# Kernel optimization log

Hardware: AMD Instinct MI355X
Metric: run time of the kernel (lower is better)

## Reference

```python
import jax, jax.numpy as jnp
import numpy as np

EPS = 1e-8


def setup_inputs() -> dict:
    key = jax.random.key(0)
    k1, k2, k3 = jax.random.split(key, 3)
    B, K, L, D = 4, 64, 128, 768
    context = jax.random.normal(k1, (B, K, 2, L, D), dtype=jnp.float32)
    # MlpModule(input_size=D): Linear(D, D) -> ReLU -> Linear(D, 1)
    w1 = jax.random.normal(k2, (D, D), dtype=jnp.float32) * (1.0 / np.sqrt(D))
    b1 = jnp.zeros((D,), dtype=jnp.float32)
    w2 = jax.random.normal(k3, (D, 1), dtype=jnp.float32) * (1.0 / np.sqrt(D))
    b2 = jnp.zeros((1,), dtype=jnp.float32)
    return {"context": context, "w1": w1, "b1": b1, "w2": w2, "b2": b2}


def reference(context, w1, b1, w2, b2):
    # context: [B, K, 2, L, D]; slice 0 = context tokens, slice 1 = entity tokens
    ctx = context[:, :, 0, :, :]   # [B, K, L, D]
    ent = context[:, :, 1, :, :]   # [B, K, L, D]

    ctx_norm = jnp.linalg.norm(ctx, axis=-1, keepdims=True)  # [B, K, L, 1]
    ent_norm = jnp.linalg.norm(ent, axis=-1, keepdims=True)  # [B, K, L, 1]

    # cosine-similarity score matrix: [B, K, L, L]
    denom = ctx_norm * jnp.swapaxes(ent_norm, -1, -2) + EPS
    scores = jnp.einsum('bkld,bkmd->bklm', ctx, ent) / denom

    # normalized embeddings (torch code does in-place /= before the stack)
    ctx_n = ctx / ctx_norm
    ent_n = ent / ent_norm

    # top-1 match along entity axis, gather matched entity token per context token
    argmax_idx = jnp.argmax(scores, axis=-1)                       # [B, K, L] int
    matched = jnp.take_along_axis(ent_n, argmax_idx[..., None], axis=2)  # [B, K, L, D]

    pair = jnp.stack([ctx_n, matched], axis=-2)  # [B, K, L, 2, D]

    # MLP: Linear(D,D) -> ReLU -> Linear(D,1), then sum over the pair axis
    h = jax.nn.relu(jnp.einsum('bklpd,de->bklpe', pair, w1) + b1)
    out = jnp.einsum('bklpd,do->bklpo', h, w2) + b2   # [B, K, L, 2, 1]
    out = jnp.sum(out, axis=-2)                        # [B, K, L, 1]
    return jnp.squeeze(out, axis=-1)                   # [B, K, L]
```

## Files before the change

### kernel.cpp

```cpp
#include <hip/hip_runtime.h>
#include <hip/hip_bf16.h>
#include <stdint.h>

#define NB 4
#define NK 64
#define NL 128
#define ND 768
#define NBK (NB*NK)
#define NROW (NBK*NL)
#define LD2 (NL*ND)
#define EPSF 1e-8f
#define THETA 2e-3f
#define CAP 16384

#define TSTR 40

typedef __bf16 bf16x8 __attribute__((ext_vector_type(8)));
typedef float  f32x4  __attribute__((ext_vector_type(4)));

__device__ __forceinline__ int row_off(int r) {
  if (r < NROW) return r*ND + (r >> 7)*LD2;
  int r2 = r - NROW;
  return r2*ND + (r2 >> 7)*LD2 + LD2;
}

__global__ __launch_bounds__(256) void k0_w1t(const float* __restrict__ w1,
                                              __bf16* __restrict__ w1t,
                                              unsigned long long* __restrict__ amax2,
                                              unsigned* __restrict__ cntg) {
  __shared__ float tile[64][68];
  int idx = blockIdx.x*256 + threadIdx.x;
  if (idx < NROW) amax2[idx] = 0ull;
  if (idx == 0) *cntg = 0u;
  int kb = (blockIdx.x / 12) * 64, eb = (blockIdx.x % 12) * 64;
  int t = threadIdx.x;
  int r = t >> 2, c0 = (t & 3) * 16;
  #pragma unroll
  for (int j = 0; j < 4; j++) {
    f32x4 v = *(const f32x4*)(w1 + (kb + r)*ND + eb + c0 + j*4);
    *(f32x4*)&tile[r][c0 + j*4] = v;
  }
  __syncthreads();
  int e = t & 63, gi = t >> 6;
  int eg = eb + e;
  #pragma unroll
  for (int g2 = 0; g2 < 2; g2++) {
    int g = gi*2 + g2;
    bf16x8 o;
    #pragma unroll
    for (int j = 0; j < 8; j++) o[j] = (__bf16)tile[g*8 + j][e];
    int G = (kb >> 3) + (g ^ (eg & 7));
    *(bf16x8*)(w1t + eg*ND + G*8) = o;
  }
}

__device__ __forceinline__ void cvt4(f32x4 v, unsigned& hp0, unsigned& hp1,
                                     unsigned& lp0, unsigned& lp1, float& sq) {
  unsigned u0 = __float_as_uint(v[0]), u1 = __float_as_uint(v[1]);
  unsigned u2 = __float_as_uint(v[2]), u3 = __float_as_uint(v[3]);
  hp0 = (u1 & 0xffff0000u) | (u0 >> 16);
  hp1 = (u3 & 0xffff0000u) | (u2 >> 16);
  float l0 = v[0] - __uint_as_float(u0 & 0xffff0000u);
  float l1 = v[1] - __uint_as_float(u1 & 0xffff0000u);
  float l2 = v[2] - __uint_as_float(u2 & 0xffff0000u);
  float l3 = v[3] - __uint_as_float(u3 & 0xffff0000u);
  lp0 = (__float_as_uint(l1) & 0xffff0000u) | (__float_as_uint(l0) >> 16);
  lp1 = (__float_as_uint(l3) & 0xffff0000u) | (__float_as_uint(l2) >> 16);
  sq += v[0]*v[0] + v[1]*v[1] + v[2]*v[2] + v[3]*v[3];
}

__device__ __forceinline__ bf16x8 rnd8(f32x4 a, f32x4 b) {
  bf16x8 o;
  o[0] = (__bf16)a[0]; o[1] = (__bf16)a[1]; o[2] = (__bf16)a[2]; o[3] = (__bf16)a[3];
  o[4] = (__bf16)b[0]; o[5] = (__bf16)b[1]; o[6] = (__bf16)b[2]; o[7] = (__bf16)b[3];
  return o;
}

__global__ __launch_bounds__(512) void k2a_screen(
    const float* __restrict__ ctxall, float* __restrict__ norm,
    int* __restrict__ amax, unsigned* __restrict__ cntg,
    unsigned* __restrict__ list, __bf16* __restrict__ abf16) {
  __shared__ alignas(16) __bf16 tiles[2][4][128*TSTR];
  __shared__ float einv_s[128];
  int bk = blockIdx.x;
  int t = threadIdx.x;
  int mat = t >> 8, row = (t >> 1) & 127, kh = (t & 1) * 16;
  const float* src = ctxall + bk*2*LD2 + mat*LD2 + row*ND + kh;
  int w = t >> 6, lane = t & 63, quad = lane >> 4, eloc = lane & 15;
  __bf16* arow = abf16 ? (abf16 + (size_t)((mat ? NROW : 0) + bk*NL + row)*ND + kh)
                       : (__bf16*)0;

  f32x4 pv[4];
  #pragma unroll
  for (int i = 0; i < 4; i++) pv[i] = *(const f32x4*)(src + i*4);
  float sq = 0.f;
  f32x4 acc[8];
  #pragma unroll
  for (int ct = 0; ct < 8; ct++) acc[ct] = (f32x4){0,0,0,0};

  int p = 0;
  for (int kt = 0; kt < 24; kt++) {
    unsigned h0,h1,h2,h3, l0,l1,l2,l3;
    cvt4(pv[0], h0, h1, l0, l1, sq);
    cvt4(pv[1], h2, h3, l2, l3, sq);
    __bf16* hdst = &tiles[p][2*mat  ][row*TSTR + kh];
    __bf16* ldst = &tiles[p][2*mat+1][row*TSTR + kh];
    *(uint4*)hdst = make_uint4(h0,h1,h2,h3);
    *(uint4*)ldst = make_uint4(l0,l1,l2,l3);
    bf16x8 rb0, rb1;
    if (arow) rb0 = rnd8(pv[0], pv[1]);
    cvt4(pv[2], h0, h1, l0, l1, sq);
    cvt4(pv[3], h2, h3, l2, l3, sq);
    *((uint4*)hdst + 1) = make_uint4(h0,h1,h2,h3);
    *((uint4*)ldst + 1) = make_uint4(l0,l1,l2,l3);
    if (arow) rb1 = rnd8(pv[2], pv[3]);
    __syncthreads();
    if (arow) {
      *(bf16x8*)(arow + kt*32) = rb0;
      *(bf16x8*)(arow + kt*32 + 8) = rb1;
    }
    if (kt < 23) {
      const float* s2 = src + (kt+1)*32;
      #pragma unroll
      for (int i = 0; i < 4; i++) pv[i] = *(const f32x4*)(s2 + i*4);
    }
    bf16x8 ah = *(const bf16x8*)&tiles[p][0][(w*16+eloc)*TSTR + quad*8];
    bf16x8 al = *(const bf16x8*)&tiles[p][1][(w*16+eloc)*TSTR + quad*8];
    #pragma unroll
    for (int ct = 0; ct < 8; ct++) {
      bf16x8 bh = *(const bf16x8*)&tiles[p][2][(ct*16+eloc)*TSTR + quad*8];
      bf16x8 bl = *(const bf16x8*)&tiles[p][3][(ct*16+eloc)*TSTR + quad*8];
      acc[ct] = __builtin_amdgcn_mfma_f32_16x16x32_bf16(al, bh, acc[ct], 0, 0, 0);
      acc[ct] = __builtin_amdgcn_mfma_f32_16x16x32_bf16(ah, bl, acc[ct], 0, 0, 0);
      acc[ct] = __builtin_amdgcn_mfma_f32_16x16x32_bf16(ah, bh, acc[ct], 0, 0, 0);
    }
    p ^= 1;
  }

  float stot = sq + __shfl_xor(sq, 1);
  if ((t & 1) == 0) {
    float n = sqrtf(stot);
    if (mat == 0) norm[bk*NL + row] = n;
    else { norm[NROW + bk*NL + row] = n; einv_s[row] = 1.0f / n; }
  }
  __syncthreads();

  #pragma unroll
  for (int rr = 0; rr < 4; rr++) {
    float sc[8];
    float best = -3.0e38f; int bcol = 0;
    #pragma unroll
    for (int ct = 0; ct < 8; ct++) {
      sc[ct] = acc[ct][rr] * einv_s[ct*16 + eloc];
      int col = ct*16 + eloc;
      if (sc[ct] > best) { best = sc[ct]; bcol = col; }
    }
    #pragma unroll
    for (int m = 1; m < 16; m <<= 1) {
      float ov = __shfl_xor(best, m);
      int   oc = __shfl_xor(bcol, m);
      if (ov > best || (ov == best && oc < bcol)) { best = ov; bcol = oc; }
    }
    int grow = bk*NL + w*16 + quad*4 + rr;
    if (eloc == 0) amax[grow] = bcol;
    int cnt = 0;
    #pragma unroll
    for (int ct = 0; ct < 8; ct++) cnt += (sc[ct] >= best - THETA) ? 1 : 0;
    #pragma unroll
    for (int m = 1; m < 16; m <<= 1) cnt += __shfl_xor(cnt, m);
    if (cnt >= 2) {
      #pragma unroll
      for (int ct = 0; ct < 8; ct++) {
        if (sc[ct] >= best - THETA) {
          unsigned idx = atomicAdd(cntg, 1u);
          if (idx < CAP) list[idx] = ((unsigned)grow << 7) | (unsigned)(ct*16 + eloc);
        }
      }
    }
  }
}

__global__ __launch_bounds__(256) void k2b_rescore(
    const float* __restrict__ ctxall, const float* __restrict__ norm,
    const unsigned* __restrict__ cntg, const unsigned* __restrict__ list,
    unsigned long long* __restrict__ amax2) {
  unsigned n = *cntg; if (n > CAP) n = CAP;
  int lane = threadIdx.x & 63;
  unsigned wv = blockIdx.x*4 + (threadIdx.x >> 6);
  for (unsigned e = wv; e < n; e += 256) {
    unsigned ent = list[e];
    int row = (int)(ent >> 7), col = (int)(ent & 127);
    int bk = row >> 7;
    const float* a = ctxall + row_off(row);
    const float* b = ctxall + bk*2*LD2 + LD2 + col*ND;
    float d = 0.f;
    #pragma unroll
    for (int i = 0; i < 3; i++) {
      f32x4 va = *(const f32x4*)(a + lane*12 + i*4);
      f32x4 vb = *(const f32x4*)(b + lane*12 + i*4);
      d += va[0]*vb[0] + va[1]*vb[1] + va[2]*vb[2] + va[3]*vb[3];
    }
    #pragma unroll
    for (int m = 1; m < 64; m <<= 1) d += __shfl_xor(d, m);
    if (lane == 0) {
      float cn = norm[row], en = norm[NROW + bk*NL + col];
      float s = d / (cn*en + EPSF);
      unsigned su = __float_as_uint(s);
      unsigned ord = (su & 0x80000000u) ? ~su : (su | 0x80000000u);
      unsigned long long key = ((unsigned long long)ord << 32) | (unsigned)(127 - col);
      atomicMax(&amax2[row], key);
    }
  }
}

__global__ __launch_bounds__(256, 2) void k3_mlp_b(
    const __bf16* __restrict__ abf16, const float* __restrict__ norm,
    const __bf16* __restrict__ w1t, const float* __restrict__ b1,
    const float* __restrict__ w2, float* __restrict__ val) {
  __shared__ alignas(16) __bf16 btile[2][16*768];
  int tid = threadIdx.x;
  int wave = tid >> 6, lane = tid & 63;
  int quad = lane >> 4, eloc = lane & 15;
  int rbase = blockIdx.x*128 + wave*32;

  #pragma unroll
  for (int i = 0; i < 6; i++) {
    __builtin_amdgcn_global_load_lds(
      (const __attribute__((address_space(1))) unsigned int*)(w1t + (i*256 + tid)*8),
      (__attribute__((address_space(3))) unsigned int*)(&btile[0][0] + (i*256 + tid)*8),
      16, 0, 0);
  }

  bf16x8 afrag[2][24];
  float rinvv[2][4];
  #pragma unroll
  for (int s = 0; s < 2; s++) {
    const __bf16* src = abf16 + (size_t)(rbase + s*16 + eloc)*ND + quad*8;
    #pragma unroll
    for (int ks = 0; ks < 24; ks++)
      afrag[s][ks] = *(const bf16x8*)(src + ks*32);
    #pragma unroll
    for (int rr = 0; rr < 4; rr++)
      rinvv[s][rr] = 1.0f / norm[rbase + s*16 + quad*4 + rr];
  }

  float oacc[2][4] = {{0,0,0,0},{0,0,0,0}};
  int p = 0;
  for (int nt = 0; nt < 48; nt++) {
    __syncthreads();
    if (nt < 47) {
      const __bf16* gsrc = w1t + (nt+1)*16*ND;
      #pragma unroll
      for (int i = 0; i < 6; i++) {
        __builtin_amdgcn_global_load_lds(
          (const __attribute__((address_space(1))) unsigned int*)(gsrc + (i*256 + tid)*8),
          (__attribute__((address_space(3))) unsigned int*)(&btile[p^1][0] + (i*256 + tid)*8),
          16, 0, 0);
      }
    }
    f32x4 h0 = {0,0,0,0}, h1 = {0,0,0,0};
    #pragma unroll
    for (int ks = 0; ks < 24; ks++) {
      int g = ks*4 + quad;
      bf16x8 bfrag = *(const bf16x8*)(&btile[p][0] + eloc*ND + ((g ^ (eloc & 7))*8));
      h0 = __builtin_amdgcn_mfma_f32_16x16x32_bf16(afrag[0][ks], bfrag, h0, 0, 0, 0);
      h1 = __builtin_amdgcn_mfma_f32_16x16x32_bf16(afrag[1][ks], bfrag, h1, 0, 0, 0);
    }
    float b1v = b1[nt*16 + eloc];
    float w2v = w2[nt*16 + eloc];
    #pragma unroll
    for (int rr = 0; rr < 4; rr++) {
      oacc[0][rr] += fmaxf(h0[rr]*rinvv[0][rr] + b1v, 0.f) * w2v;
      oacc[1][rr] += fmaxf(h1[rr]*rinvv[1][rr] + b1v, 0.f) * w2v;
    }
    p ^= 1;
  }
  #pragma unroll
  for (int m = 1; m < 16; m <<= 1)
    #pragma unroll
    for (int s = 0; s < 2; s++)
      #pragma unroll
      for (int rr = 0; rr < 4; rr++)
        oacc[s][rr] += __shfl_xor(oacc[s][rr], m);
  if (eloc == 0) {
    #pragma unroll
    for (int s = 0; s < 2; s++)
      #pragma unroll
      for (int rr = 0; rr < 4; rr++)
        val[rbase + s*16 + quad*4 + rr] = oacc[s][rr];
  }
}

__global__ __launch_bounds__(256, 2) void k3_mlp(
    const float* __restrict__ ctxall, const float* __restrict__ norm,
    const __bf16* __restrict__ w1t, const float* __restrict__ b1,
    const float* __restrict__ w2, float* __restrict__ val) {
  __shared__ alignas(16) __bf16 btile[2][16*768];
  int tid = threadIdx.x;
  int wave = tid >> 6, lane = tid & 63;
  int quad = lane >> 4, eloc = lane & 15;
  int rbase = blockIdx.x*128 + wave*32;

  #pragma unroll
  for (int i = 0; i < 6; i++) {
    __builtin_amdgcn_global_load_lds(
      (const __attribute__((address_space(1))) unsigned int*)(w1t + (i*256 + tid)*8),
      (__attribute__((address_space(3))) unsigned int*)(&btile[0][0] + (i*256 + tid)*8),
      16, 0, 0);
  }

  bf16x8 afrag[2][24];
  #pragma unroll
  for (int s = 0; s < 2; s++) {
    int r = rbase + s*16 + eloc;
    const float* src = ctxall + row_off(r);
    float rinv = 1.0f / norm[r];
    #pragma unroll
    for (int ks = 0; ks < 24; ks++) {
      const float* sp = src + ks*32 + quad*8;
      f32x4 v0 = *(const f32x4*)sp;
      f32x4 v1 = *(const f32x4*)(sp + 4);
      bf16x8 a;
      a[0] = (__bf16)(v0[0]*rinv); a[1] = (__bf16)(v0[1]*rinv);
      a[2] = (__bf16)(v0[2]*rinv); a[3] = (__bf16)(v0[3]*rinv);
      a[4] = (__bf16)(v1[0]*rinv); a[5] = (__bf16)(v1[1]*rinv);
      a[6] = (__bf16)(v1[2]*rinv); a[7] = (__bf16)(v1[3]*rinv);
      afrag[s][ks] = a;
    }
  }

  float oacc[2][4] = {{0,0,0,0},{0,0,0,0}};
  int p = 0;
  for (int nt = 0; nt < 48; nt++) {
    __syncthreads();
    if (nt < 47) {
      const __bf16* gsrc = w1t + (nt+1)*16*ND;
      #pragma unroll
      for (int i = 0; i < 6; i++) {
        __builtin_amdgcn_global_load_lds(
          (const __attribute__((address_space(1))) unsigned int*)(gsrc + (i*256 + tid)*8),
          (__attribute__((address_space(3))) unsigned int*)(&btile[p^1][0] + (i*256 + tid)*8),
          16, 0, 0);
      }
    }
    f32x4 h0 = {0,0,0,0}, h1 = {0,0,0,0};
    #pragma unroll
    for (int ks = 0; ks < 24; ks++) {
      int g = ks*4 + quad;
      bf16x8 bfrag = *(const bf16x8*)(&btile[p][0] + eloc*ND + ((g ^ (eloc & 7))*8));
      h0 = __builtin_amdgcn_mfma_f32_16x16x32_bf16(afrag[0][ks], bfrag, h0, 0, 0, 0);
      h1 = __builtin_amdgcn_mfma_f32_16x16x32_bf16(afrag[1][ks], bfrag, h1, 0, 0, 0);
    }
    float b1v = b1[nt*16 + eloc];
    float w2v = w2[nt*16 + eloc];
    #pragma unroll
    for (int rr = 0; rr < 4; rr++) {
      oacc[0][rr] += fmaxf(h0[rr] + b1v, 0.f) * w2v;
      oacc[1][rr] += fmaxf(h1[rr] + b1v, 0.f) * w2v;
    }
    p ^= 1;
  }
  #pragma unroll
  for (int m = 1; m < 16; m <<= 1)
    #pragma unroll
    for (int s = 0; s < 2; s++)
      #pragma unroll
      for (int rr = 0; rr < 4; rr++)
        oacc[s][rr] += __shfl_xor(oacc[s][rr], m);
  if (eloc == 0) {
    #pragma unroll
    for (int s = 0; s < 2; s++)
      #pragma unroll
      for (int rr = 0; rr < 4; rr++)
        val[rbase + s*16 + quad*4 + rr] = oacc[s][rr];
  }
}

__global__ void k4_out(const float* __restrict__ val, const int* __restrict__ amax,
                       const unsigned long long* __restrict__ amax2,
                       const float* __restrict__ b2, float* __restrict__ out) {
  int i = blockIdx.x*256 + threadIdx.x;
  int bk = i >> 7;
  unsigned long long k = amax2[i];
  int a = k ? (127 - (int)(k & 127ull)) : amax[i];
  out[i] = val[i] + val[NROW + bk*NL + a] + 2.0f*b2[0];
}

extern "C" void kernel_launch(void* const* d_in, const int* in_sizes, int n_in,
                              void* d_out, int out_size, void* d_ws, size_t ws_size,
                              hipStream_t stream) {
  const float* ctxall = (const float*)d_in[0];
  const float* w1 = (const float*)d_in[1];
  const float* b1 = (const float*)d_in[2];
  const float* w2 = (const float*)d_in[3];
  const float* b2 = (const float*)d_in[4];
  float* out = (float*)d_out;

  char* ws = (char*)d_ws;
  float*    norm = (float*)ws;
  int*      amax = (int*)(ws + 262144);
  float*    val  = (float*)(ws + 393216);
  __bf16*   w1t  = (__bf16*)(ws + 655360);
  unsigned long long* amax2 = (unsigned long long*)(ws + 1835008);
  unsigned* cntg = (unsigned*)(ws + 2097152);
  unsigned* list = (unsigned*)(ws + 2097156);

  const size_t abf_off = 8ull << 20;
  const size_t abf_bytes = (size_t)2*NROW*ND*sizeof(__bf16);
  __bf16* abf16 = (ws_size >= abf_off + abf_bytes) ? (__bf16*)(ws + abf_off)
                                                   : (__bf16*)0;

  hipLaunchKernelGGL(k0_w1t,     dim3(144),        dim3(256), 0, stream, w1, w1t, amax2, cntg);
  hipLaunchKernelGGL(k2a_screen, dim3(NBK),        dim3(512), 0, stream, ctxall, norm, amax, cntg, list, abf16);
  hipLaunchKernelGGL(k2b_rescore,dim3(64),         dim3(256), 0, stream, ctxall, norm, cntg, list, amax2);
  if (abf16) {
    hipLaunchKernelGGL(k3_mlp_b, dim3(2*NROW/128), dim3(256), 0, stream, abf16, norm, w1t, b1, w2, val);
  } else {
    hipLaunchKernelGGL(k3_mlp,   dim3(2*NROW/128), dim3(256), 0, stream, ctxall, norm, w1t, b1, w2, val);
  }
  hipLaunchKernelGGL(k4_out,     dim3(NROW/256),   dim3(256), 0, stream, val, amax, amax2, b2, out);
}
```

Before: 441.2 us.

## Restructure bf16 MLP kernel to stream activations through LDS and hold W1 per wave

The bf16 MLP kernel is rewritten with 512 threads. Each of 8 waves owns 96 output columns, and W1 fragments are read straight from global memory (L2). The 128 activation rows are streamed through double-buffered LDS in 32-wide K slices, where before W1 tiles were streamed through LDS and A was held in registers. Accumulators for all 128 rows by 96 columns live in registers (48 f32x4 per lane), and a cross-wave LDS reduction then forms the final score. This aims to cut the redundant streaming of W1 per block and improve MFMA density, but adds heavy register pressure, per-k-step barriers and uncached W1 global loads.

```diff
diff --git a/kernel.cpp b/kernel.cpp
--- a/kernel.cpp
+++ b/kernel.cpp
@@ -12,7 +12,6 @@
 #define EPSF 1e-8f
 #define THETA 2e-3f
 #define CAP 16384
-
 #define TSTR 40
 
 typedef __bf16 bf16x8 __attribute__((ext_vector_type(8)));
@@ -213,81 +212,109 @@
   }
 }
 
-__global__ __launch_bounds__(256, 2) void k3_mlp_b(
+__global__ __launch_bounds__(512, 2) void k3_mlp_c(
     const __bf16* __restrict__ abf16, const float* __restrict__ norm,
     const __bf16* __restrict__ w1t, const float* __restrict__ b1,
     const float* __restrict__ w2, float* __restrict__ val) {
-  __shared__ alignas(16) __bf16 btile[2][16*768];
+  __shared__ alignas(16) __bf16 atile[2][128*32];
+  __shared__ float red[8][128];
   int tid = threadIdx.x;
   int wave = tid >> 6, lane = tid & 63;
   int quad = lane >> 4, eloc = lane & 15;
-  int rbase = blockIdx.x*128 + wave*32;
-
+  int rbase = blockIdx.x * 128;
+  int arow = tid >> 2, acol = (tid & 3) * 8;
+
+  {
+    const __bf16* s0 = abf16 + (size_t)(rbase + arow)*ND + acol;
+    __builtin_amdgcn_global_load_lds(
+      (const __attribute__((address_space(1))) unsigned int*)s0,
+      (__attribute__((address_space(3))) unsigned int*)(&atile[0][0] + tid*8),
+      16, 0, 0);
+  }
+
+  float b1v[6], w2v[6];
   #pragma unroll
   for (int i = 0; i < 6; i++) {
-    __builtin_amdgcn_global_load_lds(
-      (const __attribute__((address_space(1))) unsigned int*)(w1t + (i*256 + tid)*8),
-      (__attribute__((address_space(3))) unsigned int*)(&btile[0][0] + (i*256 + tid)*8),
-      16, 0, 0);
-  }
-
-  bf16x8 afrag[2][24];
-  float rinvv[2][4];
-  #pragma unroll
-  for (int s = 0; s < 2; s++) {
-    const __bf16* src = abf16 + (size_t)(rbase + s*16 + eloc)*ND + quad*8;
-    #pragma unroll
-    for (int ks = 0; ks < 24; ks++)
-      afrag[s][ks] = *(const bf16x8*)(src + ks*32);
-    #pragma unroll
-    for (int rr = 0; rr < 4; rr++)
-      rinvv[s][rr] = 1.0f / norm[rbase + s*16 + quad*4 + rr];
-  }
-
-  float oacc[2][4] = {{0,0,0,0},{0,0,0,0}};
+    int out = (wave + 8*i)*16 + eloc;
+    b1v[i] = b1[out];
+    w2v[i] = w2[out];
+  }
+
+  f32x4 acc[6][8];
+  #pragma unroll
+  for (int i = 0; i < 6; i++)
+    #pragma unroll
+    for (int rt = 0; rt < 8; rt++) acc[i][rt] = (f32x4){0,0,0,0};
+
   int p = 0;
-  for (int nt = 0; nt < 48; nt++) {
+  for (int ksp = 0; ksp < 12; ksp++) {
+    int ks0 = ksp*2;
     __syncthreads();
-    if (nt < 47) {
-      const __bf16* gsrc = w1t + (nt+1)*16*ND;
-      #pragma unroll
-      for (int i = 0; i < 6; i++) {
-        __builtin_amdgcn_global_load_lds(
-          (const __attribute__((address_space(1))) unsigned int*)(gsrc + (i*256 + tid)*8),
-          (__attribute__((address_space(3))) unsigned int*)(&btile[p^1][0] + (i*256 + tid)*8),
-          16, 0, 0);
-      }
-    }
-    f32x4 h0 = {0,0,0,0}, h1 = {0,0,0,0};
-    #pragma unroll
-    for (int ks = 0; ks < 24; ks++) {
-      int g = ks*4 + quad;
-      bf16x8 bfrag = *(const bf16x8*)(&btile[p][0] + eloc*ND + ((g ^ (eloc & 7))*8));
-      h0 = __builtin_amdgcn_mfma_f32_16x16x32_bf16(afrag[0][ks], bfrag, h0, 0, 0, 0);
-      h1 = __builtin_amdgcn_mfma_f32_16x16x32_bf16(afrag[1][ks], bfrag, h1, 0, 0, 0);
-    }
-    float b1v = b1[nt*16 + eloc];
-    float w2v = w2[nt*16 + eloc];
-    #pragma unroll
-    for (int rr = 0; rr < 4; rr++) {
-      oacc[0][rr] += fmaxf(h0[rr]*rinvv[0][rr] + b1v, 0.f) * w2v;
-      oacc[1][rr] += fmaxf(h1[rr]*rinvv[1][rr] + b1v, 0.f) * w2v;
+    {
+      const __bf16* s1 = abf16 + (size_t)(rbase + arow)*ND + (ks0+1)*32 + acol;
+      __builtin_amdgcn_global_load_lds(
+        (const __attribute__((address_space(1))) unsigned int*)s1,
+        (__attribute__((address_space(3))) unsigned int*)(&atile[p^1][0] + tid*8),
+        16, 0, 0);
+    }
+    bf16x8 bf0[6], bf1[6];
+    #pragma unroll
+    for (int i = 0; i < 6; i++) {
+      const __bf16* brow = w1t + ((wave + 8*i)*16 + eloc)*ND;
+      int g0 = ks0*4 + quad;
+      bf0[i] = *(const bf16x8*)(brow + ((g0       ^ (eloc & 7))*8));
+      bf1[i] = *(const bf16x8*)(brow + (((g0 + 4) ^ (eloc & 7))*8));
+    }
+    #pragma unroll
+    for (int rt = 0; rt < 8; rt++) {
+      bf16x8 af = *(const bf16x8*)&atile[p][(rt*16 + eloc)*32 + quad*8];
+      #pragma unroll
+      for (int i = 0; i < 6; i++)
+        acc[i][rt] = __builtin_amdgcn_mfma_f32_16x16x32_bf16(af, bf0[i], acc[i][rt], 0, 0, 0);
     }
     p ^= 1;
-  }
-  #pragma unroll
-  for (int m = 1; m < 16; m <<= 1)
-    #pragma unroll
-    for (int s = 0; s < 2; s++)
-      #pragma unroll
-      for (int rr = 0; rr < 4; rr++)
-        oacc[s][rr] += __shfl_xor(oacc[s][rr], m);
-  if (eloc == 0) {
-    #pragma unroll
-    for (int s = 0; s < 2; s++)
-      #pragma unroll
-      for (int rr = 0; rr < 4; rr++)
-        val[rbase + s*16 + quad*4 + rr] = oacc[s][rr];
+    __syncthreads();
+    if (ksp < 11) {
+      const __bf16* s2 = abf16 + (size_t)(rbase + arow)*ND + (ks0+2)*32 + acol;
+      __builtin_amdgcn_global_load_lds(
+        (const __attribute__((address_space(1))) unsigned int*)s2,
+        (__attribute__((address_space(3))) unsigned int*)(&atile[p^1][0] + tid*8),
+        16, 0, 0);
+    }
+    #pragma unroll
+    for (int rt = 0; rt < 8; rt++) {
+      bf16x8 af = *(const bf16x8*)&atile[p][(rt*16 + eloc)*32 + quad*8];
+      #pragma unroll
+      for (int i = 0; i < 6; i++)
+        acc[i][rt] = __builtin_amdgcn_mfma_f32_16x16x32_bf16(af, bf1[i], acc[i][rt], 0, 0, 0);
+    }
+    p ^= 1;
+  }
+
+  #pragma unroll
+  for (int rt = 0; rt < 8; rt++) {
+    f32x4 nv = *(const f32x4*)&norm[rbase + rt*16 + quad*4];
+    f32x4 rv;
+    #pragma unroll
+    for (int r = 0; r < 4; r++) rv[r] = 1.0f / nv[r];
+    f32x4 s = {0,0,0,0};
+    #pragma unroll
+    for (int i = 0; i < 6; i++)
+      #pragma unroll
+      for (int r = 0; r < 4; r++)
+        s[r] += fmaxf(acc[i][rt][r]*rv[r] + b1v[i], 0.f) * w2v[i];
+    #pragma unroll
+    for (int m = 1; m < 16; m <<= 1)
+      #pragma unroll
+      for (int r = 0; r < 4; r++) s[r] += __shfl_xor(s[r], m);
+    if (eloc == 0) *(f32x4*)&red[wave][rt*16 + quad*4] = s;
+  }
+  __syncthreads();
+  if (tid < 128) {
+    float tsum = 0.f;
+    #pragma unroll
+    for (int wv = 0; wv < 8; wv++) tsum += red[wv][tid];
+    val[rbase + tid] = tsum;
   }
 }
 
@@ -414,7 +441,7 @@
   hipLaunchKernelGGL(k2a_screen, dim3(NBK),        dim3(512), 0, stream, ctxall, norm, amax, cntg, list, abf16);
   hipLaunchKernelGGL(k2b_rescore,dim3(64),         dim3(256), 0, stream, ctxall, norm, cntg, list, amax2);
   if (abf16) {
-    hipLaunchKernelGGL(k3_mlp_b, dim3(2*NROW/128), dim3(256), 0, stream, abf16, norm, w1t, b1, w2, val);
+    hipLaunchKernelGGL(k3_mlp_c, dim3(2*NROW/128), dim3(512), 0, stream, abf16, norm, w1t, b1, w2, val);
   } else {
     hipLaunchKernelGGL(k3_mlp,   dim3(2*NROW/128), dim3(256), 0, stream, ctxall, norm, w1t, b1, w2, val);
   }
```

After: 460.0 us. 1.04x slower.
